# Performance work log

Measured on AMD Instinct MI355X. Metric: run time of the kernel, lower is better.

## Reference

```python
import jax, jax.numpy as jnp
import numpy as np

MARGIN = 0.3
NEG_FALLBACK = 1e6  # value used when a row has no negatives


def setup_inputs() -> dict:
    key = jax.random.key(0)
    k1, k2 = jax.random.split(key)
    N, D, NUM_IDS = 8192, 256, 512
    feat = jax.random.normal(k1, (N, D), dtype=jnp.float32)
    labels = jax.random.randint(k2, (N,), 0, NUM_IDS, dtype=jnp.int64)
    return {"feat": feat, "labels": labels}


def reference(feat, labels):
    N = feat.shape[0]
    sq_norms = jnp.sum(feat * feat, axis=1)  # [N]
    sq = sq_norms[:, None] + sq_norms[None, :] - 2.0 * (feat @ feat.T)  # [N,N]
    sq = jnp.maximum(sq, 0.0)
    # safe sqrt (zero distance on the diagonal would otherwise give nan grads)
    dist = jnp.where(sq > 0, jnp.sqrt(jnp.where(sq > 0, sq, 1.0)), 0.0)

    same = labels[:, None] == labels[None, :]          # [N,N] bool
    eye = jnp.eye(N, dtype=bool)
    is_pos = same & ~eye                                # exclude self-pair
    is_neg = ~same

    # hard mining: per-row masked max over positives / min over negatives
    dist_ap = jnp.where(is_pos.any(axis=1),
                        jnp.where(is_pos, dist, -jnp.inf).max(axis=1), 0.0)
    dist_an = jnp.where(is_neg.any(axis=1),
                        jnp.where(is_neg, dist, jnp.inf).min(axis=1), NEG_FALLBACK)

    # MarginRankingLoss with y=1: mean(relu(margin - (dist_an - dist_ap)))
    return jnp.mean(jnp.maximum(0.0, MARGIN + dist_ap - dist_an))
```

## Files before the change

### kernel.cpp

```cpp
#include <hip/hip_runtime.h>


constexpr int N = 8192;
constexpr int D = 256;
constexpr float MARGIN = 0.3f;
constexpr float NEG_FALLBACK = 1e6f;
constexpr float TBIG = 1e30f;

typedef __attribute__((ext_vector_type(8))) __bf16 bf16x8;
typedef __attribute__((ext_vector_type(4))) float f32x4;

__device__ __forceinline__ unsigned enc_f(float f) {
  unsigned u = __float_as_uint(f);
  return (u >> 31) ? ~u : (u | 0x80000000u);
}
__device__ __forceinline__ float dec_f(unsigned e) {
  unsigned u = (e >> 31) ? (e ^ 0x80000000u) : ~e;
  return __uint_as_float(u);
}

__device__ __forceinline__ unsigned short f2bf_rtn(float x) {
  unsigned u = __float_as_uint(x);
  return (unsigned short)((u + 0x7fffu + ((u >> 16) & 1u)) >> 16);
}


__global__ void tl_pass0f(const float* __restrict__ feat, float* __restrict__ norms,
                          unsigned* __restrict__ ap, unsigned* __restrict__ an,
                          unsigned short* __restrict__ P, float* __restrict__ out) {
  int row = blockIdx.x * 4 + (threadIdx.x >> 6);
  int lane = threadIdx.x & 63;
  float4 f = reinterpret_cast<const float4*>(feat + (size_t)row * D)[lane];
  ushort4 h;
  h.x = f2bf_rtn(f.x); h.y = f2bf_rtn(f.y); h.z = f2bf_rtn(f.z); h.w = f2bf_rtn(f.w);
  reinterpret_cast<ushort4*>(P + (size_t)row * D)[lane] = h;
  float s = fmaf(f.x, f.x, fmaf(f.y, f.y, fmaf(f.z, f.z, f.w * f.w)));
#pragma unroll
  for (int off = 32; off > 0; off >>= 1) s += __shfl_down(s, off, 64);
  if (lane == 0) {
    norms[row] = s;
    ap[row] = enc_f(-TBIG);
    an[row] = enc_f(TBIG);
  }
  if (row == 0 && lane == 0) out[0] = 0.0f;
}

__global__ __launch_bounds__(256, 3)
void tl_pass1m(const unsigned short* __restrict__ P, const int* __restrict__ labels,
               const float* __restrict__ norms,
               unsigned* __restrict__ ap, unsigned* __restrict__ an) {
  __shared__ unsigned short lA[128 * 64];
  __shared__ unsigned short lB[128 * 64];

  const int tid = threadIdx.x;
  const int wave = tid >> 6;
  const int lane = tid & 63;
  const int c = lane & 15;
  const int q = lane >> 4;
  const int ib0 = blockIdx.y * 128;
  const int jb0 = blockIdx.x * 128;
  const int wi = (wave & 1) * 64;
  const int wj = (wave >> 1) * 64;

  f32x4 acc[4][4];
#pragma unroll
  for (int a = 0; a < 4; ++a)
#pragma unroll
    for (int b = 0; b < 4; ++b) acc[a][b] = (f32x4){0.f, 0.f, 0.f, 0.f};

  const int rsub = lane >> 3;
  const int gsw = (lane & 7) ^ (rsub & 7);

  for (int kc = 0; kc < D; kc += 64) {
#pragma unroll
    for (int t = 0; t < 4; ++t) {
      int rA = wave * 32 + t * 8;
      const unsigned short* gA = P + (size_t)(ib0 + rA + rsub) * D + kc + gsw * 8;
      __builtin_amdgcn_global_load_lds(
          (const __attribute__((address_space(1))) void*)gA,
          (__attribute__((address_space(3))) void*)&lA[rA * 64], 16, 0, 0);
      const unsigned short* gB = P + (size_t)(jb0 + rA + rsub) * D + kc + gsw * 8;
      __builtin_amdgcn_global_load_lds(
          (const __attribute__((address_space(1))) void*)gB,
          (__attribute__((address_space(3))) void*)&lB[rA * 64], 16, 0, 0);
    }
    __syncthreads();

#pragma unroll
    for (int ks = 0; ks < 2; ++ks) {
      bf16x8 af[4], bfr[4];
      const int gsel = ((ks * 4 + q) ^ (c & 7)) * 8;
#pragma unroll
      for (int a = 0; a < 4; ++a)
        af[a] = *(const bf16x8*)&lA[(wi + a * 16 + c) * 64 + gsel];
#pragma unroll
      for (int b = 0; b < 4; ++b)
        bfr[b] = *(const bf16x8*)&lB[(wj + b * 16 + c) * 64 + gsel];
#pragma unroll
      for (int a = 0; a < 4; ++a)
#pragma unroll
        for (int b = 0; b < 4; ++b)
          acc[a][b] = __builtin_amdgcn_mfma_f32_16x16x32_bf16(af[a], bfr[b], acc[a][b], 0, 0, 0);
    }
    __syncthreads();
  }

  int cj[4]; float nj[4]; int lj[4];
#pragma unroll
  for (int b = 0; b < 4; ++b) {
    cj[b] = jb0 + wj + b * 16 + c;
    nj[b] = norms[cj[b]];
    lj[b] = labels[cj[b]];
  }

  float* redAP = (float*)lA;
  float* redAN = ((float*)lA) + 256;

#pragma unroll
  for (int a = 0; a < 4; ++a) {
#pragma unroll
    for (int r = 0; r < 4; ++r) {
      int rg = ib0 + wi + a * 16 + q * 4 + r;
      int li = labels[rg];
      float tp = -TBIG, tn = TBIG;
#pragma unroll
      for (int b = 0; b < 4; ++b) {
        float t = fmaf(-2.f, acc[a][b][r], nj[b]);
        if (lj[b] == li) {
          if (cj[b] != rg) tp = fmaxf(tp, t);
        } else {
          tn = fminf(tn, t);
        }
      }
#pragma unroll
      for (int m = 1; m < 16; m <<= 1) {
        tp = fmaxf(tp, __shfl_xor(tp, m, 64));
        tn = fminf(tn, __shfl_xor(tn, m, 64));
      }
      if (c == 0) {
        int rl = wi + a * 16 + q * 4 + r;
        redAP[rl * 2 + (wave >> 1)] = tp;
        redAN[rl * 2 + (wave >> 1)] = tn;
      }
    }
  }
  __syncthreads();
  if (tid < 128) {
    float tp = fmaxf(redAP[tid * 2], redAP[tid * 2 + 1]);
    float tn = fminf(redAN[tid * 2], redAN[tid * 2 + 1]);
    atomicMax(&ap[ib0 + tid], enc_f(tp));
    atomicMin(&an[ib0 + tid], enc_f(tn));
  }
}

__global__ void tl_pass2f(const unsigned* __restrict__ ap, const unsigned* __restrict__ an,
                          const float* __restrict__ norms, float* __restrict__ out) {
  int r = blockIdx.x * 256 + threadIdx.x;
  float ni = norms[r];
  float tp = dec_f(ap[r]);
  float tn = dec_f(an[r]);
  float dap = (tp < -1e29f) ? 0.f : sqrtf(fmaxf(ni + tp, 0.f));
  float dan = (tn > 1e29f) ? NEG_FALLBACK : sqrtf(fmaxf(ni + tn, 0.f));
  float v = fmaxf(0.f, MARGIN + dap - dan) * (1.0f / (float)N);
#pragma unroll
  for (int off = 32; off > 0; off >>= 1) v += __shfl_down(v, off, 64);
  __shared__ float red[4];
  int lane = threadIdx.x & 63, w = threadIdx.x >> 6;
  if (lane == 0) red[w] = v;
  __syncthreads();
  if (threadIdx.x == 0) atomicAdd(out, red[0] + red[1] + red[2] + red[3]);
}


constexpr int FB_BK = 32;
constexpr int FB_JSPLIT = 8;
constexpr int FB_JRANGE = N / FB_JSPLIT;
constexpr int FB_LDS = 132;

__global__ void tl_pass0_fb(const float* __restrict__ feat, float* __restrict__ norms,
                            float* __restrict__ ap, float* __restrict__ an,
                            float* __restrict__ out) {
  int row = blockIdx.x * 4 + (threadIdx.x >> 6);
  int lane = threadIdx.x & 63;
  float4 f = reinterpret_cast<const float4*>(feat + (size_t)row * D)[lane];
  float s = f.x * f.x + f.y * f.y + f.z * f.z + f.w * f.w;
#pragma unroll
  for (int off = 32; off > 0; off >>= 1) s += __shfl_down(s, off, 64);
  if (lane == 0) { norms[row] = s; ap[row] = 0.0f; an[row] = NEG_FALLBACK; }
  if (row == 0 && lane == 0) out[0] = 0.0f;
}

__global__ __launch_bounds__(256, 2)
void tl_pass1_fb(const float* __restrict__ feat, const int* __restrict__ labels,
                 const float* __restrict__ norms,
                 unsigned int* __restrict__ ap, unsigned int* __restrict__ an) {
  __shared__ float As[FB_BK][FB_LDS];
  __shared__ float Bs[FB_BK][FB_LDS];
  const int tid = threadIdx.x;
  const int tx = tid & 15, ty = tid >> 4;
  const int ib0 = blockIdx.y * 128;
  const int jbase = blockIdx.x * FB_JRANGE;
  float ni[8]; int li[8]; int ri[8];
#pragma unroll
  for (int a = 0; a < 8; ++a) {
    int r = ty * 4 + (a & 3) + ((a >> 2) << 6);
    ri[a] = ib0 + r; ni[a] = norms[ri[a]]; li[a] = labels[ri[a]];
  }
  float apv[8], anv[8];
#pragma unroll
  for (int a = 0; a < 8; ++a) { apv[a] = 0.0f; anv[a] = NEG_FALLBACK; }
  for (int jt = 0; jt < FB_JRANGE; jt += 128) {
    const int jb = jbase + jt;
    float acc[8][8];
#pragma unroll
    for (int a = 0; a < 8; ++a)
#pragma unroll
      for (int b = 0; b < 8; ++b) acc[a][b] = 0.0f;
    for (int kc = 0; kc < D; kc += FB_BK) {
#pragma unroll
      for (int u = 0; u < 4; ++u) {
        int lin = tid + u * 256;
        int row = lin >> 3, c4 = lin & 7;
        float4 va = *reinterpret_cast<const float4*>(feat + (size_t)(ib0 + row) * D + kc + c4 * 4);
        As[c4 * 4 + 0][row] = va.x; As[c4 * 4 + 1][row] = va.y;
        As[c4 * 4 + 2][row] = va.z; As[c4 * 4 + 3][row] = va.w;
        float4 vb = *reinterpret_cast<const float4*>(feat + (size_t)(jb + row) * D + kc + c4 * 4);
        Bs[c4 * 4 + 0][row] = vb.x; Bs[c4 * 4 + 1][row] = vb.y;
        Bs[c4 * 4 + 2][row] = vb.z; Bs[c4 * 4 + 3][row] = vb.w;
      }
      __syncthreads();
#pragma unroll 8
      for (int k = 0; k < FB_BK; ++k) {
        float4 a0 = *reinterpret_cast<const float4*>(&As[k][ty * 4]);
        float4 a1 = *reinterpret_cast<const float4*>(&As[k][64 + ty * 4]);
        float4 b0 = *reinterpret_cast<const float4*>(&Bs[k][tx * 4]);
        float4 b1 = *reinterpret_cast<const float4*>(&Bs[k][64 + tx * 4]);
        float av[8] = {a0.x, a0.y, a0.z, a0.w, a1.x, a1.y, a1.z, a1.w};
        float bv[8] = {b0.x, b0.y, b0.z, b0.w, b1.x, b1.y, b1.z, b1.w};
#pragma unroll
        for (int a = 0; a < 8; ++a)
#pragma unroll
          for (int b = 0; b < 8; ++b) acc[a][b] = fmaf(av[a], bv[b], acc[a][b]);
      }
      __syncthreads();
    }
#pragma unroll
    for (int b = 0; b < 8; ++b) {
      int cjx = jb + tx * 4 + (b & 3) + ((b >> 2) << 6);
      float njx = norms[cjx]; int ljx = labels[cjx];
#pragma unroll
      for (int a = 0; a < 8; ++a) {
        float sq = fmaxf(ni[a] + njx - 2.0f * acc[a][b], 0.0f);
        float dist = sqrtf(sq);
        if (li[a] == ljx) { if (ri[a] != cjx) apv[a] = fmaxf(apv[a], dist); }
        else anv[a] = fminf(anv[a], dist);
      }
    }
  }
  __syncthreads();
  float* red = &As[0][0];
#pragma unroll
  for (int a = 0; a < 8; ++a) {
    int r = ty * 4 + (a & 3) + ((a >> 2) << 6);
    red[r * 16 + tx] = apv[a];
  }
  __syncthreads();
  if (tid < 128) {
    float m = red[tid * 16];
#pragma unroll
    for (int t = 1; t < 16; ++t) m = fmaxf(m, red[tid * 16 + t]);
    atomicMax(&ap[ib0 + tid], __float_as_uint(m));
  }
  __syncthreads();
#pragma unroll
  for (int a = 0; a < 8; ++a) {
    int r = ty * 4 + (a & 3) + ((a >> 2) << 6);
    red[r * 16 + tx] = anv[a];
  }
  __syncthreads();
  if (tid < 128) {
    float m = red[tid * 16];
#pragma unroll
    for (int t = 1; t < 16; ++t) m = fminf(m, red[tid * 16 + t]);
    atomicMin(&an[ib0 + tid], __float_as_uint(m));
  }
}

__global__ void tl_pass2_fb(const float* __restrict__ ap, const float* __restrict__ an,
                            float* __restrict__ out) {
  int r = blockIdx.x * 256 + threadIdx.x;
  float v = fmaxf(0.0f, MARGIN + ap[r] - an[r]) * (1.0f / (float)N);
#pragma unroll
  for (int off = 32; off > 0; off >>= 1) v += __shfl_down(v, off, 64);
  __shared__ float red[4];
  int lane = threadIdx.x & 63, w = threadIdx.x >> 6;
  if (lane == 0) red[w] = v;
  __syncthreads();
  if (threadIdx.x == 0) atomicAdd(out, red[0] + red[1] + red[2] + red[3]);
}


extern "C" void kernel_launch(void* const* d_in, const int* in_sizes, int n_in,
                              void* d_out, int out_size, void* d_ws, size_t ws_size,
                              hipStream_t stream) {
  const float* feat = (const float*)d_in[0];
  const int* labels = (const int*)d_in[1];
  float* out = (float*)d_out;

  float* norms = (float*)d_ws;
  unsigned* ap = (unsigned*)(norms + N);
  unsigned* an = ap + N;
  unsigned short* P = (unsigned short*)(an + N);
  const size_t NEED = 3 * (size_t)N * 4 + (size_t)N * D * 2;

  if (ws_size >= NEED) {
    tl_pass0f<<<N / 4, 256, 0, stream>>>(feat, norms, ap, an, P, out);
    dim3 grid1(N / 128, N / 128);
    tl_pass1m<<<grid1, 256, 0, stream>>>(P, labels, norms, ap, an);
    tl_pass2f<<<N / 256, 256, 0, stream>>>(ap, an, norms, out);
  } else {
    float* apf = (float*)ap;
    float* anf = (float*)an;
    tl_pass0_fb<<<N / 4, 256, 0, stream>>>(feat, norms, apf, anf, out);
    dim3 grid1(FB_JSPLIT, N / 128);
    tl_pass1_fb<<<grid1, 256, 0, stream>>>(feat, labels, norms, (unsigned*)apf, (unsigned*)anf);
    tl_pass2_fb<<<N / 256, 256, 0, stream>>>(apf, anf, out);
  }
}
```

Before: 126.7 us.

## Keep row tile resident in LDS and stream eight column tiles per block

Each block now loads its 128-row A tile (full K) into LDS once and loops over eight 128-column tiles. B fragments are read straight from global memory into registers with a double-buffered prefetch, and hard-positive/negative minima and maxima are kept in registers across tiles. The grid shrinks eightfold and the cross-wave LDS reduction is replaced by direct atomics. This removes repeated A loads, most barriers and many atomics, at the cost of uncoalesced, L2-dependent B loads, higher register pressure (launch bounds lowered to 2 blocks/CU) and dropping the explicit self-pair exclusion for positives.

```diff
diff --git a/kernel.cpp b/kernel.cpp
--- a/kernel.cpp
+++ b/kernel.cpp
@@ -18,7 +18,6 @@
   unsigned u = (e >> 31) ? (e ^ 0x80000000u) : ~e;
   return __uint_as_float(u);
 }
-
 __device__ __forceinline__ unsigned short f2bf_rtn(float x) {
   unsigned u = __float_as_uint(x);
   return (unsigned short)((u + 0x7fffu + ((u >> 16) & 1u)) >> 16);
@@ -45,12 +44,12 @@
   if (row == 0 && lane == 0) out[0] = 0.0f;
 }
 
-__global__ __launch_bounds__(256, 3)
+
+__global__ __launch_bounds__(256, 2)
 void tl_pass1m(const unsigned short* __restrict__ P, const int* __restrict__ labels,
                const float* __restrict__ norms,
                unsigned* __restrict__ ap, unsigned* __restrict__ an) {
-  __shared__ unsigned short lA[128 * 64];
-  __shared__ unsigned short lB[128 * 64];
+  __shared__ unsigned short lA[4][128][64];
 
   const int tid = threadIdx.x;
   const int wave = tid >> 6;
@@ -58,109 +57,124 @@
   const int c = lane & 15;
   const int q = lane >> 4;
   const int ib0 = blockIdx.y * 128;
-  const int jb0 = blockIdx.x * 128;
+  const int jbase = blockIdx.x * 1024;
   const int wi = (wave & 1) * 64;
   const int wj = (wave >> 1) * 64;
 
-  f32x4 acc[4][4];
-#pragma unroll
-  for (int a = 0; a < 4; ++a)
-#pragma unroll
-    for (int b = 0; b < 4; ++b) acc[a][b] = (f32x4){0.f, 0.f, 0.f, 0.f};
-
   const int rsub = lane >> 3;
   const int gsw = (lane & 7) ^ (rsub & 7);
-
-  for (int kc = 0; kc < D; kc += 64) {
+#pragma unroll
+  for (int kc = 0; kc < 4; ++kc) {
 #pragma unroll
     for (int t = 0; t < 4; ++t) {
       int rA = wave * 32 + t * 8;
-      const unsigned short* gA = P + (size_t)(ib0 + rA + rsub) * D + kc + gsw * 8;
+      const unsigned short* gA = P + (size_t)(ib0 + rA + rsub) * D + kc * 64 + gsw * 8;
       __builtin_amdgcn_global_load_lds(
           (const __attribute__((address_space(1))) void*)gA,
-          (__attribute__((address_space(3))) void*)&lA[rA * 64], 16, 0, 0);
-      const unsigned short* gB = P + (size_t)(jb0 + rA + rsub) * D + kc + gsw * 8;
-      __builtin_amdgcn_global_load_lds(
-          (const __attribute__((address_space(1))) void*)gB,
-          (__attribute__((address_space(3))) void*)&lB[rA * 64], 16, 0, 0);
-    }
-    __syncthreads();
-
-#pragma unroll
-    for (int ks = 0; ks < 2; ++ks) {
-      bf16x8 af[4], bfr[4];
-      const int gsel = ((ks * 4 + q) ^ (c & 7)) * 8;
+          (__attribute__((address_space(3))) void*)&lA[kc][rA][0], 16, 0, 0);
+    }
+  }
+
+  int li[4][4];
+#pragma unroll
+  for (int a = 0; a < 4; ++a)
+#pragma unroll
+    for (int r = 0; r < 4; ++r)
+      li[a][r] = labels[ib0 + wi + a * 16 + q * 4 + r];
+
+  float tp[4][4], tn[4][4];
+#pragma unroll
+  for (int a = 0; a < 4; ++a)
+#pragma unroll
+    for (int r = 0; r < 4; ++r) { tp[a][r] = -TBIG; tn[a][r] = TBIG; }
+
+  __syncthreads();
+
+  bf16x8 bb[2][4];
+#pragma unroll
+  for (int b = 0; b < 4; ++b)
+    bb[0][b] = *(const bf16x8*)(P + (size_t)(jbase + wj + b * 16 + c) * D + q * 8);
+
+  for (int jt = 0; jt < 8; ++jt) {
+    const int jb = jbase + jt * 128;
+    float njv[4]; int ljv[4];
+#pragma unroll
+    for (int b = 0; b < 4; ++b) {
+      int cjb = jb + wj + b * 16 + c;
+      njv[b] = norms[cjb];
+      ljv[b] = labels[cjb];
+    }
+
+    f32x4 acc[4][4];
+#pragma unroll
+    for (int a = 0; a < 4; ++a)
+#pragma unroll
+      for (int b = 0; b < 4; ++b) acc[a][b] = (f32x4){0.f, 0.f, 0.f, 0.f};
+
+#pragma unroll
+    for (int ks = 0; ks < 8; ++ks) {
+      const int pjb = (ks == 7) ? ((jt < 7) ? jb + 128 : jb) : jb;
+      const int pks = (ks == 7) ? 0 : ks + 1;
+#pragma unroll
+      for (int b = 0; b < 4; ++b)
+        bb[(ks + 1) & 1][b] =
+            *(const bf16x8*)(P + (size_t)(pjb + wj + b * 16 + c) * D + pks * 32 + q * 8);
+
+      const int kc = ks >> 1;
+      const int gsel = (((ks & 1) * 4 + q) ^ (c & 7)) * 8;
+      bf16x8 af[4];
 #pragma unroll
       for (int a = 0; a < 4; ++a)
-        af[a] = *(const bf16x8*)&lA[(wi + a * 16 + c) * 64 + gsel];
-#pragma unroll
-      for (int b = 0; b < 4; ++b)
-        bfr[b] = *(const bf16x8*)&lB[(wj + b * 16 + c) * 64 + gsel];
+        af[a] = *(const bf16x8*)&lA[kc][wi + a * 16 + c][gsel];
+
 #pragma unroll
       for (int a = 0; a < 4; ++a)
 #pragma unroll
         for (int b = 0; b < 4; ++b)
-          acc[a][b] = __builtin_amdgcn_mfma_f32_16x16x32_bf16(af[a], bfr[b], acc[a][b], 0, 0, 0);
-    }
-    __syncthreads();
-  }
-
-  int cj[4]; float nj[4]; int lj[4];
-#pragma unroll
-  for (int b = 0; b < 4; ++b) {
-    cj[b] = jb0 + wj + b * 16 + c;
-    nj[b] = norms[cj[b]];
-    lj[b] = labels[cj[b]];
-  }
-
-  float* redAP = (float*)lA;
-  float* redAN = ((float*)lA) + 256;
-
-#pragma unroll
-  for (int a = 0; a < 4; ++a) {
+          acc[a][b] = __builtin_amdgcn_mfma_f32_16x16x32_bf16(af[a], bb[ks & 1][b], acc[a][b], 0, 0, 0);
+    }
+
+#pragma unroll
+    for (int a = 0; a < 4; ++a)
+#pragma unroll
+      for (int r = 0; r < 4; ++r) {
+#pragma unroll
+        for (int b = 0; b < 4; ++b) {
+          float t = fmaf(-2.f, acc[a][b][r], njv[b]);
+          bool s = (ljv[b] == li[a][r]);
+          tp[a][r] = fmaxf(tp[a][r], s ? t : -TBIG);
+          tn[a][r] = fminf(tn[a][r], s ? TBIG : t);
+        }
+      }
+  }
+
+#pragma unroll
+  for (int a = 0; a < 4; ++a)
 #pragma unroll
     for (int r = 0; r < 4; ++r) {
-      int rg = ib0 + wi + a * 16 + q * 4 + r;
-      int li = labels[rg];
-      float tp = -TBIG, tn = TBIG;
-#pragma unroll
-      for (int b = 0; b < 4; ++b) {
-        float t = fmaf(-2.f, acc[a][b][r], nj[b]);
-        if (lj[b] == li) {
-          if (cj[b] != rg) tp = fmaxf(tp, t);
-        } else {
-          tn = fminf(tn, t);
-        }
-      }
+      float vp = tp[a][r], vn = tn[a][r];
 #pragma unroll
       for (int m = 1; m < 16; m <<= 1) {
-        tp = fmaxf(tp, __shfl_xor(tp, m, 64));
-        tn = fminf(tn, __shfl_xor(tn, m, 64));
+        vp = fmaxf(vp, __shfl_xor(vp, m, 64));
+        vn = fminf(vn, __shfl_xor(vn, m, 64));
       }
       if (c == 0) {
-        int rl = wi + a * 16 + q * 4 + r;
-        redAP[rl * 2 + (wave >> 1)] = tp;
-        redAN[rl * 2 + (wave >> 1)] = tn;
-      }
-    }
-  }
-  __syncthreads();
-  if (tid < 128) {
-    float tp = fmaxf(redAP[tid * 2], redAP[tid * 2 + 1]);
-    float tn = fminf(redAN[tid * 2], redAN[tid * 2 + 1]);
-    atomicMax(&ap[ib0 + tid], enc_f(tp));
-    atomicMin(&an[ib0 + tid], enc_f(tn));
-  }
-}
+        int row = ib0 + wi + a * 16 + q * 4 + r;
+        atomicMax(&ap[row], enc_f(vp));
+        atomicMin(&an[row], enc_f(vn));
+      }
+    }
+}
+
 
 __global__ void tl_pass2f(const unsigned* __restrict__ ap, const unsigned* __restrict__ an,
                           const float* __restrict__ norms, float* __restrict__ out) {
   int r = blockIdx.x * 256 + threadIdx.x;
   float ni = norms[r];
-  float tp = dec_f(ap[r]);
-  float tn = dec_f(an[r]);
-  float dap = (tp < -1e29f) ? 0.f : sqrtf(fmaxf(ni + tp, 0.f));
-  float dan = (tn > 1e29f) ? NEG_FALLBACK : sqrtf(fmaxf(ni + tn, 0.f));
+  float tpv = dec_f(ap[r]);
+  float tnv = dec_f(an[r]);
+  float dap = (tpv < -1e29f) ? 0.f : sqrtf(fmaxf(ni + tpv, 0.f));
+  float dan = (tnv > 1e29f) ? NEG_FALLBACK : sqrtf(fmaxf(ni + tnv, 0.f));
   float v = fmaxf(0.f, MARGIN + dap - dan) * (1.0f / (float)N);
 #pragma unroll
   for (int off = 32; off > 0; off >>= 1) v += __shfl_down(v, off, 64);
@@ -315,7 +329,7 @@
 
   if (ws_size >= NEED) {
     tl_pass0f<<<N / 4, 256, 0, stream>>>(feat, norms, ap, an, P, out);
-    dim3 grid1(N / 128, N / 128);
+    dim3 grid1(8, N / 128);
     tl_pass1m<<<grid1, 256, 0, stream>>>(P, labels, norms, ap, an);
     tl_pass2f<<<N / 256, 256, 0, stream>>>(ap, an, norms, out);
   } else {
```

After: 147.8 us. 1.17x slower.
